# Kernel optimization log

Hardware: AMD Instinct MI355X
Metric: run time of the kernel (lower is better)

Reference implementation:

```python
import jax, jax.numpy as jnp
import numpy as np

N_NODES = 25000
N_EDGES = 400000
CHANNELS = 32
EDGE_FEAT_DIM = 8
HIDDEN = 64
NUM_IRREPS = 4  # messages irreps = 2x0e + 2x1o -> 4 irreps, dim 8
AVG_NUM_NEIGHBORS = 16.0


def _mlp(x, W0, W1, W2, W3):
    # e3nn MultiLayerPerceptron: dense layers with 1/sqrt(fan_in) forward
    # normalization, silu on hidden layers, no output activation.
    for W in (W0, W1, W2):
        x = jax.nn.silu(x @ (W / jnp.sqrt(jnp.float32(W.shape[0]))))
    return x @ (W3 / jnp.sqrt(jnp.float32(W3.shape[0])))


def setup_inputs() -> dict:
    key = jax.random.key(0)
    ks = jax.random.split(key, 9)
    node_feats = jax.random.normal(ks[0], (N_NODES, CHANNELS, 4), jnp.float32)
    edge_attrs = jax.random.normal(ks[1], (N_EDGES, 4), jnp.float32)
    edge_feats = jax.random.normal(ks[2], (N_EDGES, EDGE_FEAT_DIM), jnp.float32)
    senders = jax.random.randint(ks[3], (N_EDGES,), 0, N_NODES)
    receivers = jax.random.randint(ks[4], (N_EDGES,), 0, N_NODES)
    W0 = jax.random.normal(ks[5], (EDGE_FEAT_DIM, HIDDEN), jnp.float32)
    W1 = jax.random.normal(ks[6], (HIDDEN, HIDDEN), jnp.float32)
    W2 = jax.random.normal(ks[7], (HIDDEN, HIDDEN), jnp.float32)
    W3 = jax.random.normal(ks[8], (HIDDEN, CHANNELS * NUM_IRREPS), jnp.float32)
    return {"node_feats": node_feats, "edge_attrs": edge_attrs,
            "edge_feats": edge_feats, "senders": senders, "receivers": receivers,
            "W0": W0, "W1": W1, "W2": W2, "W3": W3}


def reference(node_feats, edge_attrs, edge_feats, senders, receivers, W0, W1, W2, W3):
    # Gather sender node features: [E, C, 4] with irreps 0e (dim1) + 1o (dim3)
    x = node_feats[senders]
    s, v = x[..., 0], x[..., 1:4]            # [E,C], [E,C,3]
    a_s = edge_attrs[:, 0]                   # Y_0: [E]
    a_v = edge_attrs[:, 1:4]                 # Y_1: [E,3]

    # CG tensor product filtered to 0e + 1o (e3nn normalization: sqrt(2l3+1)*w3j)
    m0a = s * a_s[:, None]                                   # 0e x 0e -> 0e  [E,C]
    m0b = jnp.einsum('ecd,ed->ec', v, a_v) / jnp.sqrt(3.0)   # 1o x 1o -> 0e  [E,C]
    m1a = s[..., None] * a_v[:, None, :]                     # 0e x 1o -> 1o  [E,C,3]
    m1b = v * a_s[:, None, None]                             # 1o x 0e -> 1o  [E,C,3]

    # Edge MLP gate: [E, C*num_irreps] -> mul_to_axis -> [E, C, num_irreps]
    mix = _mlp(edge_feats, W0, W1, W2, W3).reshape(N_EDGES, CHANNELS, NUM_IRREPS)

    # Elementwise tensor product with 4x0e scalars: per-irrep gating
    out_s = jnp.stack([m0a * mix[..., 0], m0b * mix[..., 1]], axis=-1)          # [E,C,2]
    out_v = jnp.concatenate([m1a * mix[..., 2:3], m1b * mix[..., 3:4]], axis=-1)  # [E,C,6]
    messages = jnp.concatenate([out_s, out_v], axis=-1)                          # [E,C,8]

    # Scatter-add into receivers, then normalize by sqrt(avg_num_neighbors)
    agg = jax.ops.segment_sum(messages, receivers, num_segments=N_NODES)
    return agg / jnp.sqrt(AVG_NUM_NEIGHBORS)
```

## Files before the change

kernel.cpp:

```cpp
#include <hip/hip_runtime.h>
#include <hip/hip_fp16.h>

#define NE 400000
#define NN 25000
#define MAXDEG 56
#define LDS_STRIDE 65

typedef __attribute__((ext_vector_type(8))) _Float16 half8;
typedef __attribute__((ext_vector_type(4))) _Float16 half4;
typedef __attribute__((ext_vector_type(4))) float f32x4;

#define WS_MIX_OFF   0ull
#define WS_SLOTS_OFF 102400000ull
#define WS_CNT_OFF   108000000ull
#define WS_WBUF_OFF  108100000ull
#define WS_NEED      108136864ull

#define WB_L0 0
#define WB_L1 2048
#define WB_L2 6144
#define WB_L3 10240

__device__ __forceinline__ float fast_silu(float x) {
    float e = __expf(-x);
    return x * __builtin_amdgcn_rcpf(1.0f + e);
}

__global__ __launch_bounds__(64) void prep_weights(
    const float* __restrict__ W0, const float* __restrict__ W1,
    const float* __restrict__ W2, const float* __restrict__ W3,
    _Float16* __restrict__ wbuf)
{
    const int f    = blockIdx.x;
    const int lane = threadIdx.x;
    const int n    = lane & 15;
    const int quad = lane >> 4;

    const float* W; int K, N, kt, nt, fl, base; float scale;
    if (f < 4)       { W = W0; K = 8;  N = 64;  fl = f;      kt = 0;       nt = fl;     scale = 0.35355339059327373f; base = WB_L0; }
    else if (f < 12) { W = W1; K = 64; N = 64;  fl = f - 4;  kt = fl >> 2; nt = fl & 3; scale = 0.125f;   base = WB_L1; }
    else if (f < 20) { W = W2; K = 64; N = 64;  fl = f - 12; kt = fl >> 2; nt = fl & 3; scale = 0.125f;   base = WB_L2; }
    else             { W = W3; K = 64; N = 128; fl = f - 20; kt = fl >> 3; nt = fl & 7; scale = 0.03125f; base = WB_L3; }

    _Float16 v[8];
    #pragma unroll
    for (int j = 0; j < 8; ++j) {
        const int k = kt * 32 + quad * 8 + j;
        const float val = (k < K) ? W[k * N + nt * 16 + n] * scale : 0.0f;
        v[j] = (_Float16)val;
    }
    *(half8*)(wbuf + base + fl * 512 + lane * 8) = *(const half8*)v;
}

__global__ __launch_bounds__(256) void build_kernel(
    const int* __restrict__ receivers, int* __restrict__ cnt, int* __restrict__ slots)
{
    int e = blockIdx.x * 256 + threadIdx.x;
    if (e >= NE) return;
    int r = receivers[e];
    int s = atomicAdd(&cnt[r], 1);
    if (s < MAXDEG) slots[r * MAXDEG + s] = e;
}

#define HS 72
__global__ __launch_bounds__(256) void mlp_mfma_kernel(
    const float*    __restrict__ edge_feats,
    const _Float16* __restrict__ wbuf,
    _Float16*       __restrict__ mix16)
{
    __shared__ _Float16 H[4 * 16 * HS];
    const int wave = threadIdx.x >> 6;
    const int lane = threadIdx.x & 63;
    const int col  = lane & 15;
    const int quad = lane >> 4;
    const int e0   = (blockIdx.x * 4 + wave) * 16;

    _Float16* Hw = &H[wave * 16 * HS];
    const half8* wb = (const half8*)wbuf;
    const f32x4 zero4 = {0.f, 0.f, 0.f, 0.f};

    half8 b0 = {0, 0, 0, 0, 0, 0, 0, 0};
    if (quad == 0) {
        const float4* efp = (const float4*)(edge_feats + (size_t)(e0 + col) * 8);
        const float4 x = efp[0], y = efp[1];
        b0[0] = (_Float16)x.x; b0[1] = (_Float16)x.y; b0[2] = (_Float16)x.z; b0[3] = (_Float16)x.w;
        b0[4] = (_Float16)y.x; b0[5] = (_Float16)y.y; b0[6] = (_Float16)y.z; b0[7] = (_Float16)y.w;
    }

    {
        #pragma unroll
        for (int nt = 0; nt < 4; ++nt) {
            f32x4 acc = __builtin_amdgcn_mfma_f32_16x16x32_f16(wb[(WB_L0 / 512 + nt) * 64 + lane], b0, zero4, 0, 0, 0);
            half4 h;
            #pragma unroll
            for (int r = 0; r < 4; ++r) h[r] = (_Float16)fast_silu(acc[r]);
            *(half4*)&Hw[col * HS + nt * 16 + quad * 4] = h;
        }
    }

    #pragma unroll
    for (int layer = 0; layer < 2; ++layer) {
        const int wbase = (layer == 0 ? WB_L1 : WB_L2) / 512;
        const half8 blo = *(const half8*)&Hw[col * HS + 0  + quad * 8];
        const half8 bhi = *(const half8*)&Hw[col * HS + 32 + quad * 8];
        f32x4 acc[4];
        #pragma unroll
        for (int nt = 0; nt < 4; ++nt) {
            acc[nt] = __builtin_amdgcn_mfma_f32_16x16x32_f16(wb[(wbase + 0 + nt) * 64 + lane], blo, zero4, 0, 0, 0);
            acc[nt] = __builtin_amdgcn_mfma_f32_16x16x32_f16(wb[(wbase + 4 + nt) * 64 + lane], bhi, acc[nt], 0, 0, 0);
        }
        #pragma unroll
        for (int nt = 0; nt < 4; ++nt) {
            half4 h;
            #pragma unroll
            for (int r = 0; r < 4; ++r) h[r] = (_Float16)fast_silu(acc[nt][r]);
            *(half4*)&Hw[col * HS + nt * 16 + quad * 4] = h;
        }
    }

    {
        const half8 blo = *(const half8*)&Hw[col * HS + 0  + quad * 8];
        const half8 bhi = *(const half8*)&Hw[col * HS + 32 + quad * 8];
        _Float16* mrow = mix16 + (size_t)(e0 + col) * 128;
        #pragma unroll
        for (int nt = 0; nt < 8; ++nt) {
            f32x4 acc = __builtin_amdgcn_mfma_f32_16x16x32_f16(wb[(WB_L3 / 512 + 0 + nt) * 64 + lane], blo, zero4, 0, 0, 0);
            acc = __builtin_amdgcn_mfma_f32_16x16x32_f16(wb[(WB_L3 / 512 + 8 + nt) * 64 + lane], bhi, acc, 0, 0, 0);
            half4 h;
            #pragma unroll
            for (int r = 0; r < 4; ++r) h[r] = (_Float16)acc[r];
            *(half4*)&mrow[nt * 16 + quad * 4] = h;
        }
    }
}

__global__ __launch_bounds__(64) void gather_kernel(
    const float*    __restrict__ node_feats,
    const float*    __restrict__ edge_attrs,
    const int*      __restrict__ senders,
    const _Float16* __restrict__ mix16,
    const int*      __restrict__ cnt,
    const int*      __restrict__ slots,
    float*          __restrict__ out)
{
    const int n    = blockIdx.x;
    const int lane = threadIdx.x;
    const int g    = lane >> 4;
    const int s    = lane & 15;
    const int c0   = 2 * s;
    const float inv_sqrt3 = 0.5773502691896258f;

    int d = cnt[n];
    if (d > MAXDEG) d = MAXDEG;
    const int* sl = slots + n * MAXDEG;

    float acc[16];
    #pragma unroll
    for (int j = 0; j < 16; ++j) acc[j] = 0.0f;

    #pragma unroll 2
    for (int base = 0; base < d; base += 4) {
        const int  ei  = base + g;
        const bool act = (ei < d);
        const int  eic = act ? ei : 0;
        const int  eid = sl[eic];
        const int  snd = senders[eid];
        const float4 a4v = ((const float4*)edge_attrs)[eid];
        const half8 m8 = *(const half8*)(mix16 + (size_t)eid * 128 + c0 * 4);
        const float4 xA = ((const float4*)(node_feats + (size_t)snd * 128))[c0];
        const float4 xB = ((const float4*)(node_feats + (size_t)snd * 128))[c0 + 1];

        const float z = act ? 1.0f : 0.0f;
        const float as = a4v.x, av0 = a4v.y, av1 = a4v.z, av2 = a4v.w;

        {
            const float m0 = z * (float)m8[0], m1 = z * (float)m8[1];
            const float m2 = z * (float)m8[2], m3 = z * (float)m8[3];
            const float sc = xA.x, v0 = xA.y, v1 = xA.z, v2 = xA.w;
            acc[0] = fmaf(sc * as, m0, acc[0]);
            const float dv = v0 * av0 + v1 * av1 + v2 * av2;
            acc[1] = fmaf(dv * inv_sqrt3, m1, acc[1]);
            acc[2] = fmaf(sc * av0, m2, acc[2]);
            acc[3] = fmaf(sc * av1, m2, acc[3]);
            acc[4] = fmaf(sc * av2, m2, acc[4]);
            acc[5] = fmaf(v0 * as, m3, acc[5]);
            acc[6] = fmaf(v1 * as, m3, acc[6]);
            acc[7] = fmaf(v2 * as, m3, acc[7]);
        }
        {
            const float m0 = z * (float)m8[4], m1 = z * (float)m8[5];
            const float m2 = z * (float)m8[6], m3 = z * (float)m8[7];
            const float sc = xB.x, v0 = xB.y, v1 = xB.z, v2 = xB.w;
            acc[8]  = fmaf(sc * as, m0, acc[8]);
            const float dv = v0 * av0 + v1 * av1 + v2 * av2;
            acc[9]  = fmaf(dv * inv_sqrt3, m1, acc[9]);
            acc[10] = fmaf(sc * av0, m2, acc[10]);
            acc[11] = fmaf(sc * av1, m2, acc[11]);
            acc[12] = fmaf(sc * av2, m2, acc[12]);
            acc[13] = fmaf(v0 * as, m3, acc[13]);
            acc[14] = fmaf(v1 * as, m3, acc[14]);
            acc[15] = fmaf(v2 * as, m3, acc[15]);
        }
    }

    #pragma unroll
    for (int j = 0; j < 16; ++j) {
        acc[j] += __shfl_xor(acc[j], 16, 64);
        acc[j] += __shfl_xor(acc[j], 32, 64);
    }

    if (g == 0) {
        float4* op = (float4*)(out + (size_t)n * 256 + s * 16);
        float4 r0; r0.x = acc[0];  r0.y = acc[1];  r0.z = acc[2];  r0.w = acc[3];
        float4 r1; r1.x = acc[4];  r1.y = acc[5];  r1.z = acc[6];  r1.w = acc[7];
        float4 r2; r2.x = acc[8];  r2.y = acc[9];  r2.z = acc[10]; r2.w = acc[11];
        float4 r3; r3.x = acc[12]; r3.y = acc[13]; r3.z = acc[14]; r3.w = acc[15];
        op[0] = r0; op[1] = r1; op[2] = r2; op[3] = r3;
    }
}

__global__ __launch_bounds__(128) void edge_mp_kernel(
    const float* __restrict__ node_feats, const float* __restrict__ edge_attrs,
    const float* __restrict__ edge_feats, const int* __restrict__ senders,
    const int* __restrict__ receivers, const float* __restrict__ W0,
    const float* __restrict__ W1, const float* __restrict__ W2,
    const float* __restrict__ W3, float* __restrict__ out)
{
    __shared__ float hbuf[128 * LDS_STRIDE];
    const int tid = threadIdx.x;
    const int e   = blockIdx.x * 128 + tid;
    if (e >= NE) return;
    float* hl = &hbuf[tid * LDS_STRIDE];

    float4 ef0 = ((const float4*)edge_feats)[e * 2 + 0];
    float4 ef1 = ((const float4*)edge_feats)[e * 2 + 1];
    float ef[8] = {ef0.x, ef0.y, ef0.z, ef0.w, ef1.x, ef1.y, ef1.z, ef1.w};
    float acc[64];
    #pragma unroll
    for (int i = 0; i < 64; ++i) acc[i] = 0.0f;
    #pragma unroll
    for (int j = 0; j < 8; ++j) {
        const float xj = ef[j];
        const float* wrow = W0 + j * 64;
        #pragma unroll
        for (int i = 0; i < 64; ++i) acc[i] = fmaf(xj, wrow[i], acc[i]);
    }
    {
        const float s0 = 0.35355339059327373f;
        #pragma unroll
        for (int i = 0; i < 64; ++i) hl[i] = fast_silu(acc[i] * s0);
    }
    #pragma unroll
    for (int i = 0; i < 64; ++i) acc[i] = 0.0f;
    #pragma unroll 4
    for (int j = 0; j < 64; ++j) {
        const float xj = hl[j];
        const float* wrow = W1 + j * 64;
        #pragma unroll
        for (int i = 0; i < 64; ++i) acc[i] = fmaf(xj, wrow[i], acc[i]);
    }
    #pragma unroll
    for (int i = 0; i < 64; ++i) hl[i] = fast_silu(acc[i] * 0.125f);
    #pragma unroll
    for (int i = 0; i < 64; ++i) acc[i] = 0.0f;
    #pragma unroll 4
    for (int j = 0; j < 64; ++j) {
        const float xj = hl[j];
        const float* wrow = W2 + j * 64;
        #pragma unroll
        for (int i = 0; i < 64; ++i) acc[i] = fmaf(xj, wrow[i], acc[i]);
    }
    float h2[64];
    #pragma unroll
    for (int i = 0; i < 64; ++i) h2[i] = fast_silu(acc[i] * 0.125f);

    const int snd = senders[e];
    const int rcv = receivers[e];
    const float4 a4 = ((const float4*)edge_attrs)[e];
    const float a_s = a4.x, av0 = a4.y, av1 = a4.z, av2 = a4.w;
    const float4* nf4 = (const float4*)(node_feats + (size_t)snd * 128);
    float* outp = out + (size_t)rcv * 256;
    const float mixscale = 0.03125f;
    const float inv_sqrt3 = 0.5773502691896258f;

    #pragma unroll 2
    for (int c = 0; c < 32; ++c) {
        float m0 = 0.0f, m1 = 0.0f, m2 = 0.0f, m3 = 0.0f;
        const float* wc = W3 + c * 4;
        #pragma unroll
        for (int j = 0; j < 64; ++j) {
            const float hj = h2[j];
            m0 = fmaf(hj, wc[j * 128 + 0], m0);
            m1 = fmaf(hj, wc[j * 128 + 1], m1);
            m2 = fmaf(hj, wc[j * 128 + 2], m2);
            m3 = fmaf(hj, wc[j * 128 + 3], m3);
        }
        m0 *= mixscale; m1 *= mixscale; m2 *= mixscale; m3 *= mixscale;
        const float4 x4 = nf4[c];
        const float s = x4.x, v0 = x4.y, v1 = x4.z, v2 = x4.w;
        float* op = outp + c * 8;
        atomicAdd(op + 0, s * a_s * m0);
        const float dotva = v0 * av0 + v1 * av1 + v2 * av2;
        atomicAdd(op + 1, dotva * inv_sqrt3 * m1);
        atomicAdd(op + 2, s * av0 * m2);
        atomicAdd(op + 3, s * av1 * m2);
        atomicAdd(op + 4, s * av2 * m2);
        atomicAdd(op + 5, v0 * a_s * m3);
        atomicAdd(op + 6, v1 * a_s * m3);
        atomicAdd(op + 7, v2 * a_s * m3);
    }
}

extern "C" void kernel_launch(void* const* d_in, const int* in_sizes, int n_in,
                              void* d_out, int out_size, void* d_ws, size_t ws_size,
                              hipStream_t stream) {
    const float* node_feats = (const float*)d_in[0];
    const float* edge_attrs = (const float*)d_in[1];
    const float* edge_feats = (const float*)d_in[2];
    const int*   senders    = (const int*)d_in[3];
    const int*   receivers  = (const int*)d_in[4];
    const float* W0 = (const float*)d_in[5];
    const float* W1 = (const float*)d_in[6];
    const float* W2 = (const float*)d_in[7];
    const float* W3 = (const float*)d_in[8];
    float* outp = (float*)d_out;

    if (ws_size >= WS_NEED) {
        char* w = (char*)d_ws;
        _Float16* mix16 = (_Float16*)(w + WS_MIX_OFF);
        int*      slots = (int*)(w + WS_SLOTS_OFF);
        int*      cnt   = (int*)(w + WS_CNT_OFF);
        _Float16* wbuf  = (_Float16*)(w + WS_WBUF_OFF);

        hipMemsetAsync(cnt, 0, NN * sizeof(int), stream);
        hipLaunchKernelGGL(prep_weights, dim3(36), dim3(64), 0, stream,
                           W0, W1, W2, W3, wbuf);
        hipLaunchKernelGGL(build_kernel, dim3((NE + 255) / 256), dim3(256), 0, stream,
                           receivers, cnt, slots);
        hipLaunchKernelGGL(mlp_mfma_kernel, dim3(NE / 64), dim3(256), 0, stream,
                           edge_feats, wbuf, mix16);
        hipLaunchKernelGGL(gather_kernel, dim3(NN), dim3(64), 0, stream,
                           node_feats, edge_attrs, senders, mix16, cnt, slots, outp);
    } else {
        hipMemsetAsync(d_out, 0, (size_t)out_size * sizeof(float), stream);
        hipLaunchKernelGGL(edge_mp_kernel, dim3((NE + 127) / 128), dim3(128), 0, stream,
                           node_feats, edge_attrs, edge_feats, senders, receivers,
                           W0, W1, W2, W3, outp);
    }
}
```

Baseline: 229.4 us.

## Fuse receiver bucketing into MLP kernel, stage weights in LDS, drop memset

The counter memset moves into the weight-prep kernel, and the receiver slot-building atomics move into the MLP kernel, removing one memset and one kernel launch. Each MLP block also copies the full fp16 weight buffer into shared memory once and reads MFMA operands from there instead of from global memory in every wave. In exchange, shared memory per block rises to about 45 KB, which may lower occupancy. The atomics now run inside the MFMA kernel and may contend with its own work.

```diff
diff --git a/kernel.cpp b/kernel.cpp
--- a/kernel.cpp
+++ b/kernel.cpp
@@ -29,10 +29,13 @@
 __global__ __launch_bounds__(64) void prep_weights(
     const float* __restrict__ W0, const float* __restrict__ W1,
     const float* __restrict__ W2, const float* __restrict__ W3,
-    _Float16* __restrict__ wbuf)
+    _Float16* __restrict__ wbuf, int* __restrict__ cnt)
 {
     const int f    = blockIdx.x;
     const int lane = threadIdx.x;
+
+    for (int i = f * 64 + lane; i < NN; i += 36 * 64) cnt[i] = 0;
+
     const int n    = lane & 15;
     const int quad = lane >> 4;
 
@@ -52,32 +55,44 @@
     *(half8*)(wbuf + base + fl * 512 + lane * 8) = *(const half8*)v;
 }
 
-__global__ __launch_bounds__(256) void build_kernel(
-    const int* __restrict__ receivers, int* __restrict__ cnt, int* __restrict__ slots)
-{
-    int e = blockIdx.x * 256 + threadIdx.x;
-    if (e >= NE) return;
-    int r = receivers[e];
-    int s = atomicAdd(&cnt[r], 1);
-    if (s < MAXDEG) slots[r * MAXDEG + s] = e;
-}
-
 #define HS 72
-__global__ __launch_bounds__(256) void mlp_mfma_kernel(
+__global__ __launch_bounds__(256) void mlp_build_kernel(
     const float*    __restrict__ edge_feats,
+    const int*      __restrict__ receivers,
     const _Float16* __restrict__ wbuf,
+    int*            __restrict__ cnt,
+    int*            __restrict__ slots,
     _Float16*       __restrict__ mix16)
 {
-    __shared__ _Float16 H[4 * 16 * HS];
-    const int wave = threadIdx.x >> 6;
-    const int lane = threadIdx.x & 63;
+    __shared__ _Float16 LB[18432 + 4 * 16 * HS];
+    const int tid  = threadIdx.x;
+    const int wave = tid >> 6;
+    const int lane = tid & 63;
     const int col  = lane & 15;
     const int quad = lane >> 4;
-    const int e0   = (blockIdx.x * 4 + wave) * 16;
-
-    _Float16* Hw = &H[wave * 16 * HS];
-    const half8* wb = (const half8*)wbuf;
+
+    {
+        const half8* src = (const half8*)wbuf;
+        half8* dst = (half8*)LB;
+        #pragma unroll
+        for (int i = 0; i < 9; ++i)
+            dst[i * 256 + tid] = src[i * 256 + tid];
+    }
+
+    {
+        const int e = blockIdx.x * 256 + tid;
+        if (e < NE) {
+            const int r = receivers[e];
+            const int s = atomicAdd(&cnt[r], 1);
+            if (s < MAXDEG) slots[r * MAXDEG + s] = e;
+        }
+    }
+    __syncthreads();
+
+    const half8* wl = (const half8*)LB;
+    _Float16* Hw = LB + 18432 + wave * 16 * HS;
     const f32x4 zero4 = {0.f, 0.f, 0.f, 0.f};
+    const int e0 = (blockIdx.x * 4 + wave) * 16;
 
     half8 b0 = {0, 0, 0, 0, 0, 0, 0, 0};
     if (quad == 0) {
@@ -90,7 +105,7 @@
     {
         #pragma unroll
         for (int nt = 0; nt < 4; ++nt) {
-            f32x4 acc = __builtin_amdgcn_mfma_f32_16x16x32_f16(wb[(WB_L0 / 512 + nt) * 64 + lane], b0, zero4, 0, 0, 0);
+            f32x4 acc = __builtin_amdgcn_mfma_f32_16x16x32_f16(wl[nt * 64 + lane], b0, zero4, 0, 0, 0);
             half4 h;
             #pragma unroll
             for (int r = 0; r < 4; ++r) h[r] = (_Float16)fast_silu(acc[r]);
@@ -100,14 +115,14 @@
 
     #pragma unroll
     for (int layer = 0; layer < 2; ++layer) {
-        const int wbase = (layer == 0 ? WB_L1 : WB_L2) / 512;
+        const int wo = (layer == 0) ? 4 : 12;
         const half8 blo = *(const half8*)&Hw[col * HS + 0  + quad * 8];
         const half8 bhi = *(const half8*)&Hw[col * HS + 32 + quad * 8];
         f32x4 acc[4];
         #pragma unroll
         for (int nt = 0; nt < 4; ++nt) {
-            acc[nt] = __builtin_amdgcn_mfma_f32_16x16x32_f16(wb[(wbase + 0 + nt) * 64 + lane], blo, zero4, 0, 0, 0);
-            acc[nt] = __builtin_amdgcn_mfma_f32_16x16x32_f16(wb[(wbase + 4 + nt) * 64 + lane], bhi, acc[nt], 0, 0, 0);
+            acc[nt] = __builtin_amdgcn_mfma_f32_16x16x32_f16(wl[(wo + nt) * 64 + lane], blo, zero4, 0, 0, 0);
+            acc[nt] = __builtin_amdgcn_mfma_f32_16x16x32_f16(wl[(wo + 4 + nt) * 64 + lane], bhi, acc[nt], 0, 0, 0);
         }
         #pragma unroll
         for (int nt = 0; nt < 4; ++nt) {
@@ -124,8 +139,8 @@
         _Float16* mrow = mix16 + (size_t)(e0 + col) * 128;
         #pragma unroll
         for (int nt = 0; nt < 8; ++nt) {
-            f32x4 acc = __builtin_amdgcn_mfma_f32_16x16x32_f16(wb[(WB_L3 / 512 + 0 + nt) * 64 + lane], blo, zero4, 0, 0, 0);
-            acc = __builtin_amdgcn_mfma_f32_16x16x32_f16(wb[(WB_L3 / 512 + 8 + nt) * 64 + lane], bhi, acc, 0, 0, 0);
+            f32x4 acc = __builtin_amdgcn_mfma_f32_16x16x32_f16(wl[(20 + nt) * 64 + lane], blo, zero4, 0, 0, 0);
+            acc = __builtin_amdgcn_mfma_f32_16x16x32_f16(wl[(28 + nt) * 64 + lane], bhi, acc, 0, 0, 0);
             half4 h;
             #pragma unroll
             for (int r = 0; r < 4; ++r) h[r] = (_Float16)acc[r];
@@ -332,13 +347,10 @@
         int*      cnt   = (int*)(w + WS_CNT_OFF);
         _Float16* wbuf  = (_Float16*)(w + WS_WBUF_OFF);
 
-        hipMemsetAsync(cnt, 0, NN * sizeof(int), stream);
         hipLaunchKernelGGL(prep_weights, dim3(36), dim3(64), 0, stream,
-                           W0, W1, W2, W3, wbuf);
-        hipLaunchKernelGGL(build_kernel, dim3((NE + 255) / 256), dim3(256), 0, stream,
-                           receivers, cnt, slots);
-        hipLaunchKernelGGL(mlp_mfma_kernel, dim3(NE / 64), dim3(256), 0, stream,
-                           edge_feats, wbuf, mix16);
+                           W0, W1, W2, W3, wbuf, cnt);
+        hipLaunchKernelGGL(mlp_build_kernel, dim3(NE / 64), dim3(256), 0, stream,
+                           edge_feats, receivers, wbuf, cnt, slots, mix16);
         hipLaunchKernelGGL(gather_kernel, dim3(NN), dim3(64), 0, stream,
                            node_feats, edge_attrs, senders, mix16, cnt, slots, outp);
     } else {
```

After: 212.1 us. 7.5% less time.
